# Performance work log

Hardware: AMD Instinct MI355X
Metric: run time of the kernel (lower is better)

The kernel has to match this reference:

```python
import jax, jax.numpy as jnp
import numpy as np

HEAD_NUM = 8
QKV_DIM = 16
SQRT_EMB = 11.313708498984761  # sqrt(128)
LOGIT_CLIP = 10.0
SOFTMAX_TEMP = 0.1


def _heads(x):
    # [B, n, H*d] -> [B, H, n, d]
    b, n, _ = x.shape
    return x.reshape(b, n, HEAD_NUM, QKV_DIM).transpose(0, 2, 1, 3)


def setup_inputs() -> dict:
    key = jax.random.key(0)
    ks = jax.random.split(key, 8)
    B, P, N, E = 32, 512, 1024, 128
    s = 1.0 / np.sqrt(E)
    return {
        "encoded_last_node": jax.random.normal(ks[0], (B, P, E), jnp.float32),
        "load": jax.random.uniform(ks[1], (B, P), jnp.float32),
        "ninf_mask": jnp.zeros((B, P, N), jnp.float32),
        "encoded_nodes": jax.random.normal(ks[2], (B, N, E), jnp.float32),
        "Wq_last": jax.random.normal(ks[3], (E + 1, E), jnp.float32) * s,
        "Wk": jax.random.normal(ks[4], (E, E), jnp.float32) * s,
        "Wv": jax.random.normal(ks[5], (E, E), jnp.float32) * s,
        "Wc": jax.random.normal(ks[6], (E, E), jnp.float32) * s,
        "bc": jnp.zeros((E,), jnp.float32),
    }


def reference(encoded_last_node, load, ninf_mask, encoded_nodes, Wq_last, Wk, Wv, Wc, bc):
    # set_kv
    k = _heads(encoded_nodes @ Wk)              # [B,H,N,d]
    v = _heads(encoded_nodes @ Wv)              # [B,H,N,d]

    # forward
    input_cat = jnp.concatenate([encoded_last_node, load[:, :, None]], axis=2)  # [B,P,E+1]
    q = _heads(input_cat @ Wq_last)             # [B,H,P,d]

    score = jnp.einsum("bhpd,bhnd->bhpn", q, k) / jnp.sqrt(jnp.float32(QKV_DIM))
    score = score + ninf_mask[:, None, :, :]
    weights = jax.nn.softmax(score, axis=3)
    out = jnp.einsum("bhpn,bhnd->bhpd", weights, v)
    out_concat = out.transpose(0, 2, 1, 3).reshape(q.shape[0], q.shape[2], HEAD_NUM * QKV_DIM)
    mh_atten_out = out_concat @ Wc + bc         # [B,P,E]

    # single-head tanh-clipped scoring against encoded_nodes
    s = jnp.einsum("bpe,bne->bpn", mh_atten_out, encoded_nodes) / SQRT_EMB
    s = LOGIT_CLIP * jnp.tanh(s) + ninf_mask
    probs = jax.nn.softmax(s / SOFTMAX_TEMP, axis=2)
    return probs
```

## Files before the change

kernel.cpp:

```cpp
#include <hip/hip_runtime.h>
#include <math.h>
#include <stdint.h>

#define B_ 32
#define P_ 512
#define N_ 1024
#define E_ 128
#define H_ 8
#define D_ 16

typedef unsigned short ushort_t;
typedef __attribute__((ext_vector_type(8))) short short8;
typedef __attribute__((ext_vector_type(4))) float f32x4;

union U8 { short8 s8; uint32_t u[4]; };

__device__ __forceinline__ void fma4(float4& acc, float a, float4 w) {
  acc.x = fmaf(a, w.x, acc.x); acc.y = fmaf(a, w.y, acc.y);
  acc.z = fmaf(a, w.z, acc.z); acc.w = fmaf(a, w.w, acc.w);
}
__device__ __forceinline__ void add4(float4& acc, float4 w) {
  acc.x += w.x; acc.y += w.y; acc.z += w.z; acc.w += w.w;
}
__device__ __forceinline__ float fast_tanh(float x) {
  x = fminf(20.f, fmaxf(-20.f, x));
  float e = __expf(2.f * x);
  return (e - 1.f) / (e + 1.f);
}
__device__ __forceinline__ uint32_t f32_to_hl(float x) {
  uint32_t bits = __float_as_uint(x);
  uint32_t hi = bits >> 16;
  float rem = x - __uint_as_float(bits & 0xFFFF0000u);
  uint32_t lo = __float_as_uint(rem) >> 16;
  return hi | (lo << 16);
}

__global__ __launch_bounds__(256, 2) void gemm128(
    const float* __restrict__ A, const float* __restrict__ W,
    const float* __restrict__ ea, const float* __restrict__ ew,
    const float* __restrict__ bias, float* __restrict__ C) {
  __shared__ float As[128][33];
  __shared__ float Ws[32][128];
  const int tid = threadIdx.x;
  const size_t m0 = (size_t)blockIdx.x * 128;
  const int tr = tid >> 3, tc = tid & 7;
  const int r0 = tr * 4;
  const int c0 = tc * 16;

  float4 acc[4][4];
#pragma unroll
  for (int j = 0; j < 4; ++j)
#pragma unroll
    for (int i = 0; i < 4; ++i) acc[j][i] = make_float4(0.f, 0.f, 0.f, 0.f);

  for (int kb = 0; kb < 4; ++kb) {
    __syncthreads();
    {
      int idx = tid;
#pragma unroll
      for (int it = 0; it < 4; ++it, idx += 256) {
        int r = idx >> 3, k4 = idx & 7;
        float4 v = reinterpret_cast<const float4*>(A + (m0 + r) * 128 + kb * 32)[k4];
        As[r][k4 * 4 + 0] = v.x; As[r][k4 * 4 + 1] = v.y;
        As[r][k4 * 4 + 2] = v.z; As[r][k4 * 4 + 3] = v.w;
      }
      idx = tid;
#pragma unroll
      for (int it = 0; it < 4; ++it, idx += 256) {
        int kk = idx >> 5, c4 = idx & 31;
        reinterpret_cast<float4*>(&Ws[kk][0])[c4] =
            reinterpret_cast<const float4*>(W + (size_t)(kb * 32 + kk) * 128)[c4];
      }
    }
    __syncthreads();
#pragma unroll 8
    for (int kk = 0; kk < 32; ++kk) {
      float a0 = As[r0 + 0][kk], a1 = As[r0 + 1][kk];
      float a2 = As[r0 + 2][kk], a3 = As[r0 + 3][kk];
      const float4* wr = reinterpret_cast<const float4*>(&Ws[kk][c0]);
      float4 w0 = wr[0], w1 = wr[1], w2 = wr[2], w3 = wr[3];
      fma4(acc[0][0], a0, w0); fma4(acc[0][1], a0, w1); fma4(acc[0][2], a0, w2); fma4(acc[0][3], a0, w3);
      fma4(acc[1][0], a1, w0); fma4(acc[1][1], a1, w1); fma4(acc[1][2], a1, w2); fma4(acc[1][3], a1, w3);
      fma4(acc[2][0], a2, w0); fma4(acc[2][1], a2, w1); fma4(acc[2][2], a2, w2); fma4(acc[2][3], a2, w3);
      fma4(acc[3][0], a3, w0); fma4(acc[3][1], a3, w1); fma4(acc[3][2], a3, w2); fma4(acc[3][3], a3, w3);
    }
  }

  if (ea != nullptr) {
    const float4* ew4 = reinterpret_cast<const float4*>(ew + c0);
    float4 e0 = ew4[0], e1 = ew4[1], e2 = ew4[2], e3 = ew4[3];
#pragma unroll
    for (int j = 0; j < 4; ++j) {
      float av = ea[m0 + r0 + j];
      fma4(acc[j][0], av, e0); fma4(acc[j][1], av, e1);
      fma4(acc[j][2], av, e2); fma4(acc[j][3], av, e3);
    }
  }
  if (bias != nullptr) {
    const float4* b4 = reinterpret_cast<const float4*>(bias + c0);
    float4 b0 = b4[0], b1 = b4[1], b2 = b4[2], b3 = b4[3];
#pragma unroll
    for (int j = 0; j < 4; ++j) {
      add4(acc[j][0], b0); add4(acc[j][1], b1); add4(acc[j][2], b2); add4(acc[j][3], b3);
    }
  }
#pragma unroll
  for (int j = 0; j < 4; ++j) {
    float4* c4p = reinterpret_cast<float4*>(C + (m0 + r0 + j) * 128 + c0);
    c4p[0] = acc[j][0]; c4p[1] = acc[j][1]; c4p[2] = acc[j][2]; c4p[3] = acc[j][3];
  }
}

__global__ __launch_bounds__(256, 1) void gemm_kv(
    const float* __restrict__ A, const float* __restrict__ Wk,
    const float* __restrict__ Wv, ushort_t* __restrict__ khl,
    ushort_t* __restrict__ vthl) {
  __shared__ float As[128][33];
  __shared__ float Wks[32][128];
  __shared__ float Wvs[32][128];
  const int tid = threadIdx.x;
  const size_t m0 = (size_t)blockIdx.x * 128;
  const int tr = tid >> 3, tc = tid & 7;
  const int r0 = tr * 4;
  const int c0 = tc * 16;

  float4 acck[4][4], accv[4][4];
#pragma unroll
  for (int j = 0; j < 4; ++j)
#pragma unroll
    for (int i = 0; i < 4; ++i) {
      acck[j][i] = make_float4(0.f, 0.f, 0.f, 0.f);
      accv[j][i] = make_float4(0.f, 0.f, 0.f, 0.f);
    }

  for (int kb = 0; kb < 4; ++kb) {
    __syncthreads();
    {
      int idx = tid;
#pragma unroll
      for (int it = 0; it < 4; ++it, idx += 256) {
        int r = idx >> 3, k4 = idx & 7;
        float4 v = reinterpret_cast<const float4*>(A + (m0 + r) * 128 + kb * 32)[k4];
        As[r][k4 * 4 + 0] = v.x; As[r][k4 * 4 + 1] = v.y;
        As[r][k4 * 4 + 2] = v.z; As[r][k4 * 4 + 3] = v.w;
      }
      idx = tid;
#pragma unroll
      for (int it = 0; it < 4; ++it, idx += 256) {
        int kk = idx >> 5, c4 = idx & 31;
        reinterpret_cast<float4*>(&Wks[kk][0])[c4] =
            reinterpret_cast<const float4*>(Wk + (size_t)(kb * 32 + kk) * 128)[c4];
      }
      idx = tid;
#pragma unroll
      for (int it = 0; it < 4; ++it, idx += 256) {
        int kk = idx >> 5, c4 = idx & 31;
        reinterpret_cast<float4*>(&Wvs[kk][0])[c4] =
            reinterpret_cast<const float4*>(Wv + (size_t)(kb * 32 + kk) * 128)[c4];
      }
    }
    __syncthreads();
#pragma unroll 4
    for (int kk = 0; kk < 32; ++kk) {
      float a0 = As[r0 + 0][kk], a1 = As[r0 + 1][kk];
      float a2 = As[r0 + 2][kk], a3 = As[r0 + 3][kk];
      const float4* wkr = reinterpret_cast<const float4*>(&Wks[kk][c0]);
      const float4* wvr = reinterpret_cast<const float4*>(&Wvs[kk][c0]);
#pragma unroll
      for (int i = 0; i < 4; ++i) {
        float4 wk = wkr[i], wv = wvr[i];
        fma4(acck[0][i], a0, wk); fma4(acck[1][i], a1, wk);
        fma4(acck[2][i], a2, wk); fma4(acck[3][i], a3, wk);
        fma4(accv[0][i], a0, wv); fma4(accv[1][i], a1, wv);
        fma4(accv[2][i], a2, wv); fma4(accv[3][i], a3, wv);
      }
    }
  }

#pragma unroll
  for (int j = 0; j < 4; ++j) {
    ushort_t* krow = khl + (m0 + r0 + j) * 256;
#pragma unroll
    for (int i = 0; i < 4; ++i) {
      uint4 pk;
      pk.x = f32_to_hl(acck[j][i].x);
      pk.y = f32_to_hl(acck[j][i].y);
      pk.z = f32_to_hl(acck[j][i].z);
      pk.w = f32_to_hl(acck[j][i].w);
      *reinterpret_cast<uint4*>(krow + 2 * (c0 + 4 * i)) = pk;
    }
  }
  const int bb = (int)(m0 >> 10);
  const int nbase = (int)(m0 & 1023) + r0;
#pragma unroll
  for (int i = 0; i < 4; ++i) {
#pragma unroll
    for (int e = 0; e < 4; ++e) {
      const int c = c0 + 4 * i + e;
      const int hh = c >> 4, dd = c & 15;
      uint4 pv;
      pv.x = f32_to_hl(reinterpret_cast<const float*>(&accv[0][i])[e]);
      pv.y = f32_to_hl(reinterpret_cast<const float*>(&accv[1][i])[e]);
      pv.z = f32_to_hl(reinterpret_cast<const float*>(&accv[2][i])[e]);
      pv.w = f32_to_hl(reinterpret_cast<const float*>(&accv[3][i])[e]);
      *reinterpret_cast<uint4*>(
          vthl + (size_t)((bb * H_ + hh) * 16 + dd) * 2048 + 2 * nbase) = pv;
    }
  }
}

__global__ __launch_bounds__(256, 2) void gemm_q(
    const float* __restrict__ A, const float* __restrict__ W,
    const float* __restrict__ ea, const float* __restrict__ ew,
    ushort_t* __restrict__ qhl) {
  __shared__ float As[128][33];
  __shared__ float Ws[32][128];
  const int tid = threadIdx.x;
  const size_t m0 = (size_t)blockIdx.x * 128;
  const int tr = tid >> 3, tc = tid & 7;
  const int r0 = tr * 4;
  const int c0 = tc * 16;

  float4 acc[4][4];
#pragma unroll
  for (int j = 0; j < 4; ++j)
#pragma unroll
    for (int i = 0; i < 4; ++i) acc[j][i] = make_float4(0.f, 0.f, 0.f, 0.f);

  for (int kb = 0; kb < 4; ++kb) {
    __syncthreads();
    {
      int idx = tid;
#pragma unroll
      for (int it = 0; it < 4; ++it, idx += 256) {
        int r = idx >> 3, k4 = idx & 7;
        float4 v = reinterpret_cast<const float4*>(A + (m0 + r) * 128 + kb * 32)[k4];
        As[r][k4 * 4 + 0] = v.x; As[r][k4 * 4 + 1] = v.y;
        As[r][k4 * 4 + 2] = v.z; As[r][k4 * 4 + 3] = v.w;
      }
      idx = tid;
#pragma unroll
      for (int it = 0; it < 4; ++it, idx += 256) {
        int kk = idx >> 5, c4 = idx & 31;
        reinterpret_cast<float4*>(&Ws[kk][0])[c4] =
            reinterpret_cast<const float4*>(W + (size_t)(kb * 32 + kk) * 128)[c4];
      }
    }
    __syncthreads();
#pragma unroll 8
    for (int kk = 0; kk < 32; ++kk) {
      float a0 = As[r0 + 0][kk], a1 = As[r0 + 1][kk];
      float a2 = As[r0 + 2][kk], a3 = As[r0 + 3][kk];
      const float4* wr = reinterpret_cast<const float4*>(&Ws[kk][c0]);
      float4 w0 = wr[0], w1 = wr[1], w2 = wr[2], w3 = wr[3];
      fma4(acc[0][0], a0, w0); fma4(acc[0][1], a0, w1); fma4(acc[0][2], a0, w2); fma4(acc[0][3], a0, w3);
      fma4(acc[1][0], a1, w0); fma4(acc[1][1], a1, w1); fma4(acc[1][2], a1, w2); fma4(acc[1][3], a1, w3);
      fma4(acc[2][0], a2, w0); fma4(acc[2][1], a2, w1); fma4(acc[2][2], a2, w2); fma4(acc[2][3], a2, w3);
      fma4(acc[3][0], a3, w0); fma4(acc[3][1], a3, w1); fma4(acc[3][2], a3, w2); fma4(acc[3][3], a3, w3);
    }
  }

  {
    const float4* ew4 = reinterpret_cast<const float4*>(ew + c0);
    float4 e0 = ew4[0], e1 = ew4[1], e2 = ew4[2], e3 = ew4[3];
#pragma unroll
    for (int j = 0; j < 4; ++j) {
      float av = ea[m0 + r0 + j];
      fma4(acc[j][0], av, e0); fma4(acc[j][1], av, e1);
      fma4(acc[j][2], av, e2); fma4(acc[j][3], av, e3);
    }
  }
#pragma unroll
  for (int j = 0; j < 4; ++j) {
    ushort_t* qrow = qhl + (m0 + r0 + j) * 256;
#pragma unroll
    for (int i = 0; i < 4; ++i) {
      uint4 pq;
      pq.x = f32_to_hl(acc[j][i].x);
      pq.y = f32_to_hl(acc[j][i].y);
      pq.z = f32_to_hl(acc[j][i].z);
      pq.w = f32_to_hl(acc[j][i].w);
      *reinterpret_cast<uint4*>(qrow + 2 * (c0 + 4 * i)) = pq;
    }
  }
}

__global__ __launch_bounds__(256, 4) void attn_mfma(
    const ushort_t* __restrict__ qhl, const ushort_t* __restrict__ khl,
    const ushort_t* __restrict__ vthl, const float* __restrict__ mask,
    float* __restrict__ O) {
  const int b = blockIdx.z, h = blockIdx.y, pt = blockIdx.x;
  const int tid = threadIdx.x;
  const int w = tid >> 6, lane = tid & 63;
  const int lp = lane & 15, g = lane >> 4;
  const int p = pt * 64 + w * 16 + lp;

  __shared__ __align__(16) ushort_t Ks[64 * 40];
  __shared__ __align__(16) ushort_t VTs[16 * 136];

  uint4 qld = *reinterpret_cast<const uint4*>(
      qhl + (size_t)(b * P_ + p) * 256 + h * 32 + g * 8);
  U8 qb1u, qb2u;
  {
    uint32_t qa[4] = {qld.x, qld.y, qld.z, qld.w};
#pragma unroll
    for (int i = 0; i < 4; ++i) {
      uint32_t lo16 = qa[i] & 0xFFFFu;
      qb1u.u[i] = lo16 | (lo16 << 16);
      qb2u.u[i] = qa[i] >> 16;
    }
  }
  const short8 qb1 = qb1u.s8, qb2 = qb2u.s8;

  const float* mrow = mask + (size_t)(b * P_ + p) * N_;

  f32x4 acc_o = {0.f, 0.f, 0.f, 0.f};
  float m_run = -1e30f, l_run = 0.f;

  for (int ch = 0; ch < N_ / 64; ++ch) {
    const int n0 = ch * 64;
    __syncthreads();
    {
      const int n = tid >> 2, seg = tid & 3;
      uint4 kv = *reinterpret_cast<const uint4*>(
          khl + (size_t)(b * N_ + n0 + n) * 256 + h * 32 + seg * 8);
      *reinterpret_cast<uint4*>(Ks + n * 40 + seg * 8) = kv;
      const int d = tid >> 4, s2 = tid & 15;
      uint4 vv = *reinterpret_cast<const uint4*>(
          vthl + (size_t)((b * H_ + h) * 16 + d) * 2048 + n0 * 2 + s2 * 8);
      *reinterpret_cast<uint4*>(VTs + d * 136 + s2 * 8) = vv;
    }
    __syncthreads();

    float sv[4][4];
    float cmax = -1e30f;
#pragma unroll
    for (int tt = 0; tt < 4; ++tt) {
      short8 ka = *reinterpret_cast<const short8*>(Ks + (tt * 16 + lp) * 40 + g * 8);
      f32x4 a = {0.f, 0.f, 0.f, 0.f};
      a = __builtin_amdgcn_mfma_f32_16x16x32_bf16(ka, qb1, a, 0, 0, 0);
      a = __builtin_amdgcn_mfma_f32_16x16x32_bf16(ka, qb2, a, 0, 0, 0);
      float4 mv = *reinterpret_cast<const float4*>(mrow + n0 + tt * 16 + g * 4);
      sv[tt][0] = fmaf(a[0], 0.25f, mv.x);
      sv[tt][1] = fmaf(a[1], 0.25f, mv.y);
      sv[tt][2] = fmaf(a[2], 0.25f, mv.z);
      sv[tt][3] = fmaf(a[3], 0.25f, mv.w);
      cmax = fmaxf(cmax, fmaxf(fmaxf(sv[tt][0], sv[tt][1]), fmaxf(sv[tt][2], sv[tt][3])));
    }
    cmax = fmaxf(cmax, __shfl_xor(cmax, 16));
    cmax = fmaxf(cmax, __shfl_xor(cmax, 32));
    const float nm = fmaxf(m_run, cmax);
    const float f = __expf(m_run - nm);
    acc_o[0] *= f; acc_o[1] *= f; acc_o[2] *= f; acc_o[3] *= f;
    float ls = 0.f;
#pragma unroll
    for (int tt = 0; tt < 4; ++tt)
#pragma unroll
      for (int r = 0; r < 4; ++r) {
        float e = __expf(sv[tt][r] - nm);
        sv[tt][r] = e;
        ls += e;
      }
    ls += __shfl_xor(ls, 16);
    ls += __shfl_xor(ls, 32);
    l_run = l_run * f + ls;
    m_run = nm;

#pragma unroll
    for (int tt = 0; tt < 4; ++tt) {
      U8 pb1, pb2;
#pragma unroll
      for (int r = 0; r < 4; ++r) {
        float pv = sv[tt][r];
        uint32_t bits = __float_as_uint(pv);
        uint32_t h16 = bits >> 16;
        float rem = pv - __uint_as_float(bits & 0xFFFF0000u);
        pb1.u[r] = h16 | (h16 << 16);
        pb2.u[r] = __float_as_uint(rem) >> 16;
      }
      short8 va = *reinterpret_cast<const short8*>(VTs + lp * 136 + tt * 32 + g * 8);
      acc_o = __builtin_amdgcn_mfma_f32_16x16x32_bf16(va, pb1.s8, acc_o, 0, 0, 0);
      acc_o = __builtin_amdgcn_mfma_f32_16x16x32_bf16(va, pb2.s8, acc_o, 0, 0, 0);
    }
  }

  const float inv = 1.f / l_run;
  float4 o;
  o.x = acc_o[0] * inv; o.y = acc_o[1] * inv;
  o.z = acc_o[2] * inv; o.w = acc_o[3] * inv;
  *reinterpret_cast<float4*>(O + (size_t)(b * P_ + p) * E_ + h * 16 + g * 4) = o;
}

__global__ __launch_bounds__(256, 2) void logits_kernel(
    const float* __restrict__ mh, const float* __restrict__ enc,
    const float* __restrict__ mask, float* __restrict__ T) {
  const int b = blockIdx.z;
  const int p0 = blockIdx.y * 128;
  const int n0 = blockIdx.x * 128;
  __shared__ float As[128][33];
  __shared__ float Bs[32][132];
  const int tid = threadIdx.x;
  const int tr = tid >> 3, tc = tid & 7;
  const int r0 = tr * 4, c0 = tc * 16;
  const float* Ab = mh + ((size_t)b * P_ + p0) * E_;
  const float* Eb = enc + (size_t)b * N_ * E_;

  float4 acc[4][4];
#pragma unroll
  for (int j = 0; j < 4; ++j)
#pragma unroll
    for (int i = 0; i < 4; ++i) acc[j][i] = make_float4(0.f, 0.f, 0.f, 0.f);

  for (int kb = 0; kb < 4; ++kb) {
    __syncthreads();
    int idx = tid;
#pragma unroll
    for (int it = 0; it < 4; ++it, idx += 256) {
      int r = idx >> 3, k4 = idx & 7;
      float4 v = reinterpret_cast<const float4*>(Ab + (size_t)r * 128 + kb * 32)[k4];
      As[r][k4 * 4 + 0] = v.x; As[r][k4 * 4 + 1] = v.y;
      As[r][k4 * 4 + 2] = v.z; As[r][k4 * 4 + 3] = v.w;
    }
    idx = tid;
#pragma unroll
    for (int it = 0; it < 4; ++it, idx += 256) {
      int nn = idx >> 3, k4 = idx & 7;
      float4 v = reinterpret_cast<const float4*>(Eb + (size_t)(n0 + nn) * 128 + kb * 32)[k4];
      Bs[k4 * 4 + 0][nn] = v.x; Bs[k4 * 4 + 1][nn] = v.y;
      Bs[k4 * 4 + 2][nn] = v.z; Bs[k4 * 4 + 3][nn] = v.w;
    }
    __syncthreads();
#pragma unroll 8
    for (int kk = 0; kk < 32; ++kk) {
      float a0 = As[r0 + 0][kk], a1 = As[r0 + 1][kk];
      float a2 = As[r0 + 2][kk], a3 = As[r0 + 3][kk];
      const float4* br = reinterpret_cast<const float4*>(&Bs[kk][c0]);
      float4 w0 = br[0], w1 = br[1], w2 = br[2], w3 = br[3];
      fma4(acc[0][0], a0, w0); fma4(acc[0][1], a0, w1); fma4(acc[0][2], a0, w2); fma4(acc[0][3], a0, w3);
      fma4(acc[1][0], a1, w0); fma4(acc[1][1], a1, w1); fma4(acc[1][2], a1, w2); fma4(acc[1][3], a1, w3);
      fma4(acc[2][0], a2, w0); fma4(acc[2][1], a2, w1); fma4(acc[2][2], a2, w2); fma4(acc[2][3], a2, w3);
      fma4(acc[3][0], a3, w0); fma4(acc[3][1], a3, w1); fma4(acc[3][2], a3, w2); fma4(acc[3][3], a3, w3);
    }
  }

  const float inv_s = 0.08838834764831845f;
#pragma unroll
  for (int j = 0; j < 4; ++j) {
    const size_t prow = ((size_t)b * P_ + p0 + r0 + j) * N_ + n0 + c0;
    const float4* mk4 = reinterpret_cast<const float4*>(mask + prow);
    float4* t4 = reinterpret_cast<float4*>(T + prow);
#pragma unroll
    for (int i = 0; i < 4; ++i) {
      float4 a = acc[j][i];
      float4 mv = mk4[i];
      float4 o;
      o.x = fmaf(10.f, fast_tanh(a.x * inv_s), mv.x);
      o.y = fmaf(10.f, fast_tanh(a.y * inv_s), mv.y);
      o.z = fmaf(10.f, fast_tanh(a.z * inv_s), mv.z);
      o.w = fmaf(10.f, fast_tanh(a.w * inv_s), mv.w);
      t4[i] = o;
    }
  }
}

__global__ __launch_bounds__(256, 4) void softmax_rows(
    const float* __restrict__ T, float* __restrict__ O) {
  const size_t row = blockIdx.x;
  const int tid = threadIdx.x;
  const float4 v = reinterpret_cast<const float4*>(T + row * N_)[tid];
  float lm = fmaxf(fmaxf(v.x, v.y), fmaxf(v.z, v.w));
#pragma unroll
  for (int o = 32; o; o >>= 1) lm = fmaxf(lm, __shfl_xor(lm, o));
  __shared__ float red[8];
  const int wave = tid >> 6, lane = tid & 63;
  if (lane == 0) red[wave] = lm;
  __syncthreads();
  const float m = fmaxf(fmaxf(red[0], red[1]), fmaxf(red[2], red[3]));
  float4 w;
  w.x = __expf((v.x - m) * 10.f);
  w.y = __expf((v.y - m) * 10.f);
  w.z = __expf((v.z - m) * 10.f);
  w.w = __expf((v.w - m) * 10.f);
  float ls = w.x + w.y + w.z + w.w;
#pragma unroll
  for (int o = 32; o; o >>= 1) ls += __shfl_xor(ls, o);
  if (lane == 0) red[4 + wave] = ls;
  __syncthreads();
  const float inv = 1.f / (red[4] + red[5] + red[6] + red[7]);
  float4 o4;
  o4.x = w.x * inv; o4.y = w.y * inv; o4.z = w.z * inv; o4.w = w.w * inv;
  reinterpret_cast<float4*>(O + row * N_)[tid] = o4;
}

extern "C" void kernel_launch(void* const* d_in, const int* in_sizes, int n_in,
                              void* d_out, int out_size, void* d_ws, size_t ws_size,
                              hipStream_t stream) {
  const float* eln  = (const float*)d_in[0];
  const float* load = (const float*)d_in[1];
  const float* mask = (const float*)d_in[2];
  const float* enc  = (const float*)d_in[3];
  const float* Wq   = (const float*)d_in[4];
  const float* Wk   = (const float*)d_in[5];
  const float* Wv   = (const float*)d_in[6];
  const float* Wc   = (const float*)d_in[7];
  const float* bc   = (const float*)d_in[8];
  float* out = (float*)d_out;

  char* base = (char*)d_ws;
  ushort_t* khl  = (ushort_t*)base;
  ushort_t* vthl = (ushort_t*)(base + 16777216);
  ushort_t* qhl  = (ushort_t*)(base + 2 * 16777216);
  float* mhbuf   = (float*)(base + 2 * 16777216);
  float* tbuf    = (float*)(base + 2 * 16777216 + 8388608);
  float* abuf    = tbuf;

  gemm_kv<<<dim3(256), 256, 0, stream>>>(enc, Wk, Wv, khl, vthl);
  gemm_q<<<dim3(128), 256, 0, stream>>>(eln, Wq, load, Wq + 128 * 128, qhl);
  attn_mfma<<<dim3(P_ / 64, H_, B_), 256, 0, stream>>>(qhl, khl, vthl, mask, abuf);
  gemm128<<<dim3(128), 256, 0, stream>>>(abuf, Wc, nullptr, nullptr, bc, mhbuf);
  logits_kernel<<<dim3(8, 4, B_), 256, 0, stream>>>(mhbuf, enc, mask, tbuf);
  softmax_rows<<<dim3(16384), 256, 0, stream>>>(tbuf, out);
}
```

Baseline: 399.7 us.

## Process two query tiles per attention block and move logits GEMM to MFMA

The attention kernel now handles 128 query rows per block with two independent accumulator sets. This halves how often K/V tiles are staged into shared memory per query row and interleaves more independent MFMA work. The FP32 logits GEMM is replaced by a bf16 hi/lo split MFMA kernel that converts encoded_nodes into shared memory on the fly. The costs are higher register pressure, fewer attention blocks, and recomputing the bf16 split of enc in every p-tile block.

```diff
diff --git a/kernel.cpp b/kernel.cpp
--- a/kernel.cpp
+++ b/kernel.cpp
@@ -293,29 +293,37 @@
   const int tid = threadIdx.x;
   const int w = tid >> 6, lane = tid & 63;
   const int lp = lane & 15, g = lane >> 4;
-  const int p = pt * 64 + w * 16 + lp;
+  const int pA = pt * 128 + w * 16 + lp;
+  const int pB = pA + 64;
 
   __shared__ __align__(16) ushort_t Ks[64 * 40];
   __shared__ __align__(16) ushort_t VTs[16 * 136];
 
-  uint4 qld = *reinterpret_cast<const uint4*>(
-      qhl + (size_t)(b * P_ + p) * 256 + h * 32 + g * 8);
-  U8 qb1u, qb2u;
+  U8 qA1u, qA2u, qB1u, qB2u;
   {
-    uint32_t qa[4] = {qld.x, qld.y, qld.z, qld.w};
+    uint4 qldA = *reinterpret_cast<const uint4*>(
+        qhl + (size_t)(b * P_ + pA) * 256 + h * 32 + g * 8);
+    uint4 qldB = *reinterpret_cast<const uint4*>(
+        qhl + (size_t)(b * P_ + pB) * 256 + h * 32 + g * 8);
+    uint32_t a[4] = {qldA.x, qldA.y, qldA.z, qldA.w};
+    uint32_t c[4] = {qldB.x, qldB.y, qldB.z, qldB.w};
 #pragma unroll
     for (int i = 0; i < 4; ++i) {
-      uint32_t lo16 = qa[i] & 0xFFFFu;
-      qb1u.u[i] = lo16 | (lo16 << 16);
-      qb2u.u[i] = qa[i] >> 16;
-    }
-  }
-  const short8 qb1 = qb1u.s8, qb2 = qb2u.s8;
-
-  const float* mrow = mask + (size_t)(b * P_ + p) * N_;
-
-  f32x4 acc_o = {0.f, 0.f, 0.f, 0.f};
-  float m_run = -1e30f, l_run = 0.f;
+      uint32_t lo16 = a[i] & 0xFFFFu;
+      qA1u.u[i] = lo16 | (lo16 << 16);
+      qA2u.u[i] = a[i] >> 16;
+      uint32_t lo16b = c[i] & 0xFFFFu;
+      qB1u.u[i] = lo16b | (lo16b << 16);
+      qB2u.u[i] = c[i] >> 16;
+    }
+  }
+  const short8 qA1 = qA1u.s8, qA2 = qA2u.s8, qB1 = qB1u.s8, qB2 = qB2u.s8;
+
+  const float* mrowA = mask + (size_t)(b * P_ + pA) * N_;
+  const float* mrowB = mask + (size_t)(b * P_ + pB) * N_;
+
+  f32x4 accA = {0.f, 0.f, 0.f, 0.f}, accB = {0.f, 0.f, 0.f, 0.f};
+  float mA = -1e30f, lA = 0.f, mB = -1e30f, lB = 0.f;
 
   for (int ch = 0; ch < N_ / 64; ++ch) {
     const int n0 = ch * 64;
@@ -332,133 +340,155 @@
     }
     __syncthreads();
 
-    float sv[4][4];
-    float cmax = -1e30f;
+    float svA[4][4], svB[4][4];
+    float cmA = -1e30f, cmB = -1e30f;
 #pragma unroll
     for (int tt = 0; tt < 4; ++tt) {
       short8 ka = *reinterpret_cast<const short8*>(Ks + (tt * 16 + lp) * 40 + g * 8);
-      f32x4 a = {0.f, 0.f, 0.f, 0.f};
-      a = __builtin_amdgcn_mfma_f32_16x16x32_bf16(ka, qb1, a, 0, 0, 0);
-      a = __builtin_amdgcn_mfma_f32_16x16x32_bf16(ka, qb2, a, 0, 0, 0);
-      float4 mv = *reinterpret_cast<const float4*>(mrow + n0 + tt * 16 + g * 4);
-      sv[tt][0] = fmaf(a[0], 0.25f, mv.x);
-      sv[tt][1] = fmaf(a[1], 0.25f, mv.y);
-      sv[tt][2] = fmaf(a[2], 0.25f, mv.z);
-      sv[tt][3] = fmaf(a[3], 0.25f, mv.w);
-      cmax = fmaxf(cmax, fmaxf(fmaxf(sv[tt][0], sv[tt][1]), fmaxf(sv[tt][2], sv[tt][3])));
-    }
-    cmax = fmaxf(cmax, __shfl_xor(cmax, 16));
-    cmax = fmaxf(cmax, __shfl_xor(cmax, 32));
-    const float nm = fmaxf(m_run, cmax);
-    const float f = __expf(m_run - nm);
-    acc_o[0] *= f; acc_o[1] *= f; acc_o[2] *= f; acc_o[3] *= f;
-    float ls = 0.f;
+      f32x4 aA = {0.f, 0.f, 0.f, 0.f};
+      aA = __builtin_amdgcn_mfma_f32_16x16x32_bf16(ka, qA1, aA, 0, 0, 0);
+      aA = __builtin_amdgcn_mfma_f32_16x16x32_bf16(ka, qA2, aA, 0, 0, 0);
+      f32x4 aB = {0.f, 0.f, 0.f, 0.f};
+      aB = __builtin_amdgcn_mfma_f32_16x16x32_bf16(ka, qB1, aB, 0, 0, 0);
+      aB = __builtin_amdgcn_mfma_f32_16x16x32_bf16(ka, qB2, aB, 0, 0, 0);
+      float4 mvA = *reinterpret_cast<const float4*>(mrowA + n0 + tt * 16 + g * 4);
+      float4 mvB = *reinterpret_cast<const float4*>(mrowB + n0 + tt * 16 + g * 4);
+      svA[tt][0] = fmaf(aA[0], 0.25f, mvA.x);
+      svA[tt][1] = fmaf(aA[1], 0.25f, mvA.y);
+      svA[tt][2] = fmaf(aA[2], 0.25f, mvA.z);
+      svA[tt][3] = fmaf(aA[3], 0.25f, mvA.w);
+      svB[tt][0] = fmaf(aB[0], 0.25f, mvB.x);
+      svB[tt][1] = fmaf(aB[1], 0.25f, mvB.y);
+      svB[tt][2] = fmaf(aB[2], 0.25f, mvB.z);
+      svB[tt][3] = fmaf(aB[3], 0.25f, mvB.w);
+      cmA = fmaxf(cmA, fmaxf(fmaxf(svA[tt][0], svA[tt][1]), fmaxf(svA[tt][2], svA[tt][3])));
+      cmB = fmaxf(cmB, fmaxf(fmaxf(svB[tt][0], svB[tt][1]), fmaxf(svB[tt][2], svB[tt][3])));
+    }
+    cmA = fmaxf(cmA, __shfl_xor(cmA, 16));
+    cmB = fmaxf(cmB, __shfl_xor(cmB, 16));
+    cmA = fmaxf(cmA, __shfl_xor(cmA, 32));
+    cmB = fmaxf(cmB, __shfl_xor(cmB, 32));
+    const float nmA = fmaxf(mA, cmA), nmB = fmaxf(mB, cmB);
+    const float fA = __expf(mA - nmA), fB = __expf(mB - nmB);
+    accA[0] *= fA; accA[1] *= fA; accA[2] *= fA; accA[3] *= fA;
+    accB[0] *= fB; accB[1] *= fB; accB[2] *= fB; accB[3] *= fB;
+    float lsA = 0.f, lsB = 0.f;
 #pragma unroll
     for (int tt = 0; tt < 4; ++tt)
 #pragma unroll
       for (int r = 0; r < 4; ++r) {
-        float e = __expf(sv[tt][r] - nm);
-        sv[tt][r] = e;
-        ls += e;
-      }
-    ls += __shfl_xor(ls, 16);
-    ls += __shfl_xor(ls, 32);
-    l_run = l_run * f + ls;
-    m_run = nm;
+        float eA = __expf(svA[tt][r] - nmA);
+        float eB = __expf(svB[tt][r] - nmB);
+        svA[tt][r] = eA; lsA += eA;
+        svB[tt][r] = eB; lsB += eB;
+      }
+    lsA += __shfl_xor(lsA, 16); lsB += __shfl_xor(lsB, 16);
+    lsA += __shfl_xor(lsA, 32); lsB += __shfl_xor(lsB, 32);
+    lA = lA * fA + lsA; mA = nmA;
+    lB = lB * fB + lsB; mB = nmB;
 
 #pragma unroll
     for (int tt = 0; tt < 4; ++tt) {
-      U8 pb1, pb2;
+      U8 pA1, pA2, pB1, pB2;
 #pragma unroll
       for (int r = 0; r < 4; ++r) {
-        float pv = sv[tt][r];
-        uint32_t bits = __float_as_uint(pv);
-        uint32_t h16 = bits >> 16;
-        float rem = pv - __uint_as_float(bits & 0xFFFF0000u);
-        pb1.u[r] = h16 | (h16 << 16);
-        pb2.u[r] = __float_as_uint(rem) >> 16;
+        uint32_t ba = __float_as_uint(svA[tt][r]);
+        uint32_t ha = ba >> 16;
+        float rema = svA[tt][r] - __uint_as_float(ba & 0xFFFF0000u);
+        pA1.u[r] = ha | (ha << 16);
+        pA2.u[r] = __float_as_uint(rema) >> 16;
+        uint32_t bb2 = __float_as_uint(svB[tt][r]);
+        uint32_t hb = bb2 >> 16;
+        float remb = svB[tt][r] - __uint_as_float(bb2 & 0xFFFF0000u);
+        pB1.u[r] = hb | (hb << 16);
+        pB2.u[r] = __float_as_uint(remb) >> 16;
       }
       short8 va = *reinterpret_cast<const short8*>(VTs + lp * 136 + tt * 32 + g * 8);
-      acc_o = __builtin_amdgcn_mfma_f32_16x16x32_bf16(va, pb1.s8, acc_o, 0, 0, 0);
-      acc_o = __builtin_amdgcn_mfma_f32_16x16x32_bf16(va, pb2.s8, acc_o, 0, 0, 0);
-    }
-  }
-
-  const float inv = 1.f / l_run;
-  float4 o;
-  o.x = acc_o[0] * inv; o.y = acc_o[1] * inv;
-  o.z = acc_o[2] * inv; o.w = acc_o[3] * inv;
-  *reinterpret_cast<float4*>(O + (size_t)(b * P_ + p) * E_ + h * 16 + g * 4) = o;
-}
-
-__global__ __launch_bounds__(256, 2) void logits_kernel(
+      accA = __builtin_amdgcn_mfma_f32_16x16x32_bf16(va, pA1.s8, accA, 0, 0, 0);
+      accA = __builtin_amdgcn_mfma_f32_16x16x32_bf16(va, pA2.s8, accA, 0, 0, 0);
+      accB = __builtin_amdgcn_mfma_f32_16x16x32_bf16(va, pB1.s8, accB, 0, 0, 0);
+      accB = __builtin_amdgcn_mfma_f32_16x16x32_bf16(va, pB2.s8, accB, 0, 0, 0);
+    }
+  }
+
+  const float invA = 1.f / lA, invB = 1.f / lB;
+  float4 oA, oB;
+  oA.x = accA[0] * invA; oA.y = accA[1] * invA; oA.z = accA[2] * invA; oA.w = accA[3] * invA;
+  oB.x = accB[0] * invB; oB.y = accB[1] * invB; oB.z = accB[2] * invB; oB.w = accB[3] * invB;
+  *reinterpret_cast<float4*>(O + (size_t)(b * P_ + pA) * E_ + h * 16 + g * 4) = oA;
+  *reinterpret_cast<float4*>(O + (size_t)(b * P_ + pB) * E_ + h * 16 + g * 4) = oB;
+}
+
+__global__ __launch_bounds__(256, 4) void logits_mfma(
     const float* __restrict__ mh, const float* __restrict__ enc,
     const float* __restrict__ mask, float* __restrict__ T) {
   const int b = blockIdx.z;
-  const int p0 = blockIdx.y * 128;
-  const int n0 = blockIdx.x * 128;
-  __shared__ float As[128][33];
-  __shared__ float Bs[32][132];
+  const int p0 = blockIdx.y * 64;
+  const int nq = blockIdx.x;
   const int tid = threadIdx.x;
-  const int tr = tid >> 3, tc = tid & 7;
-  const int r0 = tr * 4, c0 = tc * 16;
-  const float* Ab = mh + ((size_t)b * P_ + p0) * E_;
-  const float* Eb = enc + (size_t)b * N_ * E_;
-
-  float4 acc[4][4];
-#pragma unroll
-  for (int j = 0; j < 4; ++j)
-#pragma unroll
-    for (int i = 0; i < 4; ++i) acc[j][i] = make_float4(0.f, 0.f, 0.f, 0.f);
-
-  for (int kb = 0; kb < 4; ++kb) {
-    __syncthreads();
-    int idx = tid;
-#pragma unroll
-    for (int it = 0; it < 4; ++it, idx += 256) {
-      int r = idx >> 3, k4 = idx & 7;
-      float4 v = reinterpret_cast<const float4*>(Ab + (size_t)r * 128 + kb * 32)[k4];
-      As[r][k4 * 4 + 0] = v.x; As[r][k4 * 4 + 1] = v.y;
-      As[r][k4 * 4 + 2] = v.z; As[r][k4 * 4 + 3] = v.w;
-    }
-    idx = tid;
-#pragma unroll
-    for (int it = 0; it < 4; ++it, idx += 256) {
-      int nn = idx >> 3, k4 = idx & 7;
-      float4 v = reinterpret_cast<const float4*>(Eb + (size_t)(n0 + nn) * 128 + kb * 32)[k4];
-      Bs[k4 * 4 + 0][nn] = v.x; Bs[k4 * 4 + 1][nn] = v.y;
-      Bs[k4 * 4 + 2][nn] = v.z; Bs[k4 * 4 + 3][nn] = v.w;
-    }
-    __syncthreads();
-#pragma unroll 8
-    for (int kk = 0; kk < 32; ++kk) {
-      float a0 = As[r0 + 0][kk], a1 = As[r0 + 1][kk];
-      float a2 = As[r0 + 2][kk], a3 = As[r0 + 3][kk];
-      const float4* br = reinterpret_cast<const float4*>(&Bs[kk][c0]);
-      float4 w0 = br[0], w1 = br[1], w2 = br[2], w3 = br[3];
-      fma4(acc[0][0], a0, w0); fma4(acc[0][1], a0, w1); fma4(acc[0][2], a0, w2); fma4(acc[0][3], a0, w3);
-      fma4(acc[1][0], a1, w0); fma4(acc[1][1], a1, w1); fma4(acc[1][2], a1, w2); fma4(acc[1][3], a1, w3);
-      fma4(acc[2][0], a2, w0); fma4(acc[2][1], a2, w1); fma4(acc[2][2], a2, w2); fma4(acc[2][3], a2, w3);
-      fma4(acc[3][0], a3, w0); fma4(acc[3][1], a3, w1); fma4(acc[3][2], a3, w2); fma4(acc[3][3], a3, w3);
-    }
-  }
-
+  const int w = tid >> 6, lane = tid & 63;
+  const int lp = lane & 15, g = lane >> 4;
+  const int p = p0 + w * 16 + lp;
+
+  __shared__ __align__(16) ushort_t Es[64 * 264];
+
+  U8 fb1[8], fb2[8];
+  {
+    const float* mrow_mh = mh + (size_t)(b * P_ + p) * E_;
+#pragma unroll
+    for (int win = 0; win < 8; ++win) {
+      float4 v = *reinterpret_cast<const float4*>(mrow_mh + win * 16 + g * 4);
+      float vv[4] = {v.x, v.y, v.z, v.w};
+#pragma unroll
+      for (int r = 0; r < 4; ++r) {
+        uint32_t bits = __float_as_uint(vv[r]);
+        uint32_t hh = bits >> 16;
+        float rem = vv[r] - __uint_as_float(bits & 0xFFFF0000u);
+        fb1[win].u[r] = hh | (hh << 16);
+        fb2[win].u[r] = __float_as_uint(rem) >> 16;
+      }
+    }
+  }
+
+  const float* mrow = mask + (size_t)(b * P_ + p) * N_ + nq * 256;
+  float* trow = T + (size_t)(b * P_ + p) * N_ + nq * 256;
   const float inv_s = 0.08838834764831845f;
-#pragma unroll
-  for (int j = 0; j < 4; ++j) {
-    const size_t prow = ((size_t)b * P_ + p0 + r0 + j) * N_ + n0 + c0;
-    const float4* mk4 = reinterpret_cast<const float4*>(mask + prow);
-    float4* t4 = reinterpret_cast<float4*>(T + prow);
-#pragma unroll
-    for (int i = 0; i < 4; ++i) {
-      float4 a = acc[j][i];
-      float4 mv = mk4[i];
+
+  for (int ch = 0; ch < 4; ++ch) {
+    const int n0g = nq * 256 + ch * 64;
+    __syncthreads();
+    {
+      int idx = tid;
+#pragma unroll
+      for (int it = 0; it < 8; ++it, idx += 256) {
+        const int r = idx >> 5, f4 = idx & 31;
+        float4 v = *reinterpret_cast<const float4*>(
+            enc + ((size_t)b * N_ + n0g + r) * E_ + f4 * 4);
+        uint4 o;
+        o.x = f32_to_hl(v.x); o.y = f32_to_hl(v.y);
+        o.z = f32_to_hl(v.z); o.w = f32_to_hl(v.w);
+        *reinterpret_cast<uint4*>(Es + r * 264 + f4 * 8) = o;
+      }
+    }
+    __syncthreads();
+
+#pragma unroll
+    for (int tt = 0; tt < 4; ++tt) {
+      f32x4 acc = {0.f, 0.f, 0.f, 0.f};
+#pragma unroll
+      for (int win = 0; win < 8; ++win) {
+        short8 ea = *reinterpret_cast<const short8*>(
+            Es + (tt * 16 + lp) * 264 + win * 32 + g * 8);
+        acc = __builtin_amdgcn_mfma_f32_16x16x32_bf16(ea, fb1[win].s8, acc, 0, 0, 0);
+        acc = __builtin_amdgcn_mfma_f32_16x16x32_bf16(ea, fb2[win].s8, acc, 0, 0, 0);
+      }
+      float4 mv = *reinterpret_cast<const float4*>(mrow + ch * 64 + tt * 16 + g * 4);
       float4 o;
-      o.x = fmaf(10.f, fast_tanh(a.x * inv_s), mv.x);
-      o.y = fmaf(10.f, fast_tanh(a.y * inv_s), mv.y);
-      o.z = fmaf(10.f, fast_tanh(a.z * inv_s), mv.z);
-      o.w = fmaf(10.f, fast_tanh(a.w * inv_s), mv.w);
-      t4[i] = o;
+      o.x = fmaf(10.f, fast_tanh(acc[0] * inv_s), mv.x);
+      o.y = fmaf(10.f, fast_tanh(acc[1] * inv_s), mv.y);
+      o.z = fmaf(10.f, fast_tanh(acc[2] * inv_s), mv.z);
+      o.w = fmaf(10.f, fast_tanh(acc[3] * inv_s), mv.w);
+      *reinterpret_cast<float4*>(trow + ch * 64 + tt * 16 + g * 4) = o;
     }
   }
 }
@@ -516,8 +546,8 @@
 
   gemm_kv<<<dim3(256), 256, 0, stream>>>(enc, Wk, Wv, khl, vthl);
   gemm_q<<<dim3(128), 256, 0, stream>>>(eln, Wq, load, Wq + 128 * 128, qhl);
-  attn_mfma<<<dim3(P_ / 64, H_, B_), 256, 0, stream>>>(qhl, khl, vthl, mask, abuf);
+  attn_mfma<<<dim3(P_ / 128, H_, B_), 256, 0, stream>>>(qhl, khl, vthl, mask, abuf);
   gemm128<<<dim3(128), 256, 0, stream>>>(abuf, Wc, nullptr, nullptr, bc, mhbuf);
-  logits_kernel<<<dim3(8, 4, B_), 256, 0, stream>>>(mhbuf, enc, mask, tbuf);
+  logits_mfma<<<dim3(4, 8, B_), 256, 0, stream>>>(mhbuf, enc, mask, tbuf);
   softmax_rows<<<dim3(16384), 256, 0, stream>>>(tbuf, out);
 }
```

After: 357.6 us. 1.12x faster.
